# Kernel tuning notes

Measured on AMD Instinct MI355X. Metric: run time of the kernel, lower is better.

The kernel has to match this reference:

```python
import jax, jax.numpy as jnp
import numpy as np

SB_EPSILON = 0.1
SB_SIZE = 1

B, S, L = 16, 256, 24


def _shift(x, axis, k):
    """y[..., i, ...] = x[..., i + k, ...], zero-padded out of range."""
    if k == 0:
        return x
    n = x.shape[axis]
    if k > 0:
        body = jax.lax.slice_in_dim(x, k, n, axis=axis)
        pad = jnp.zeros_like(jax.lax.slice_in_dim(x, 0, k, axis=axis))
        return jnp.concatenate([body, pad], axis=axis)
    k = -k
    body = jax.lax.slice_in_dim(x, 0, n - k, axis=axis)
    pad = jnp.zeros_like(jax.lax.slice_in_dim(x, 0, k, axis=axis))
    return jnp.concatenate([pad, body], axis=axis)


def setup_inputs() -> dict:
    key = jax.random.key(0)
    k1, k2 = jax.random.split(key)
    predict = jax.random.normal(k1, (B, S, S, L), dtype=jnp.float32)
    target = (jax.random.uniform(k2, (B, S, S, L)) < 0.002).astype(jnp.float32)
    # valid spans: end >= start
    tri = (jnp.arange(S)[None, :] >= jnp.arange(S)[:, None]).astype(jnp.int32)
    mask = jnp.broadcast_to(tri[None, :, :, None], (B, S, S, L)).astype(jnp.int32)
    # keep targets only on valid spans
    target = target * mask.astype(jnp.float32)
    return {"predict": predict, "target": target, "mask": mask}


def reference(predict, target, mask):
    dt = predict.dtype
    P = (target == 1).astype(dt)            # positive spans [B,S,S,L]
    M = (mask == 1).astype(dt)              # valid-span mask
    # subtract full epsilon from each positive span
    b2l = jnp.where(target == 1, target - SB_EPSILON, target)
    for dist in range(1, SB_SIZE + 1):
        eps = SB_EPSILON / (SB_SIZE * dist * 4)
        cnt = jnp.zeros_like(P)   # num valid neighbors per positive span
        add = jnp.zeros_like(P)   # smoothing mass scattered onto neighbors
        # NOTE: original code offsets neighbors by sb_size (not dist); identical for sb_size=1
        for axis, k in ((2, SB_SIZE), (2, -SB_SIZE), (1, SB_SIZE), (1, -SB_SIZE)):
            cnt = cnt + _shift(M, axis, k)          # neighbor in range and mask==1
            add = add + _shift(P, axis, -k)         # positives scattering into this cell
        b2l = b2l + eps * (add * M + P * (dist * 4 - cnt))
    # masked BCE-with-logits, mean over mask==1 elements
    x, t = predict, b2l
    bce = jnp.maximum(x, 0) - x * t + jnp.log1p(jnp.exp(-jnp.abs(x)))
    denom = jnp.sum(M)
    return jnp.sum(bce * M) / denom
```

## Files before the change

### kernel.cpp

```cpp
#include <hip/hip_runtime.h>


#define SS 256
#define LL 24

typedef float    fvec4 __attribute__((ext_vector_type(4)));
typedef unsigned uvec4 __attribute__((ext_vector_type(4)));

constexpr float    EPS4      = 0.025f;
constexpr float    INV_DENOM = 1.0f / 12632064.0f;
constexpr int      NT        = 256;
constexpr int      NB        = 2048;
constexpr unsigned PERB6     = 197376u;
constexpr unsigned TOT6      = 16u * PERB6;
constexpr unsigned STRIDE    = (unsigned)(NB * NT);
constexpr float    LOG2E     = 1.4426950408889634f;
constexpr float    LN2       = 0.6931471805599453f;

__device__ __forceinline__ int tri_prefix(int i) {
    return (i * (513 - i)) >> 1;
}

__device__ __forceinline__ int decode_q(unsigned u, int& i_out, int& j_out) {
    unsigned b = u / PERB6;
    unsigned r = u - b * PERB6;
    unsigned c = r / 6u;
    unsigned m = r - c * 6u;
    float disc = (float)(263169u - 8u * c);
    int i = (int)((513.0f - sqrtf(disc)) * 0.5f);
    if (tri_prefix(i) > (int)c) --i;
    if (tri_prefix(i + 1) <= (int)c) ++i;
    int j = i + ((int)c - tri_prefix(i));
    i_out = i;
    j_out = j;
    return (int)(((b << 8) + (unsigned)i) * 256u + (unsigned)j) * 6 + (int)m;
}

__device__ __forceinline__ float sp_part(float x) {
    float u = __builtin_amdgcn_exp2f(-LOG2E * fabsf(x));
    return fmaxf(x, 0.f) + LN2 * __builtin_amdgcn_logf(1.f + u);
}

__device__ __forceinline__ void process(const fvec4& x, const uvec4& t,
                                        int i, int j, int q,
                                        const float* __restrict__ predf,
                                        float& acc, float& corr) {
    acc += sp_part(x.x) + sp_part(x.y) + sp_part(x.z) + sp_part(x.w);

    if ((t.x | t.y | t.z | t.w) != 0u) {
        bool hasL = j > i;
        bool hasR = j < SS - 1;
        bool hasU = i > 0;
        float cnt = (hasL ? 2.f : 0.f) + (hasR ? 1.f : 0.f) + (hasU ? 1.f : 0.f);
        int ebase = q * 4;
        unsigned tu[4] = {t.x, t.y, t.z, t.w};
        float    xv[4] = {x.x, x.y, x.z, x.w};
#pragma unroll
        for (int k = 0; k < 4; ++k) {
            if (tu[k] != 0u) {
                int e = ebase + k;
                float s = 0.f;
                if (hasL) s += predf[e - LL];
                if (hasR) s += predf[e + LL];
                if (hasU) s += predf[e - LL * SS];
                if (hasL) s += predf[e + LL * SS];
                corr += fmaf(EPS4, s - xv[k] * cnt, xv[k]);
            }
        }
    }
}

__global__ __launch_bounds__(NT) void bs_flat(const fvec4* __restrict__ pred4,
                                              const uvec4* __restrict__ targ4,
                                              const float* __restrict__ predf,
                                              float* __restrict__ partial) {
    float acc  = 0.f;
    float corr = 0.f;

    unsigned u0 = blockIdx.x * NT + threadIdx.x;
    int i0, j0;
    int q0 = decode_q(u0, i0, j0);
    fvec4 x0 = __builtin_nontemporal_load(pred4 + q0);
    uvec4 t0 = __builtin_nontemporal_load(targ4 + q0);

    unsigned u1 = u0 + STRIDE;
    bool m1 = u1 < TOT6;
    int i1 = 0, j1 = 0, q1 = 0; fvec4 x1; uvec4 t1;
    if (m1) {
        q1 = decode_q(u1, i1, j1);
        x1 = __builtin_nontemporal_load(pred4 + q1);
        t1 = __builtin_nontemporal_load(targ4 + q1);
    }

    for (;;) {
        unsigned u2 = u0 + 2 * STRIDE;
        bool m2 = u2 < TOT6;
        int i2 = 0, j2 = 0, q2 = 0; fvec4 x2; uvec4 t2;
        if (m2) {
            q2 = decode_q(u2, i2, j2);
            x2 = __builtin_nontemporal_load(pred4 + q2);
            t2 = __builtin_nontemporal_load(targ4 + q2);
        }

        process(x0, t0, i0, j0, q0, predf, acc, corr);

        if (!m1) break;
        u0 = u1; q0 = q1; i0 = i1; j0 = j1; x0 = x1; t0 = t1;
        u1 = u2; q1 = q2; i1 = i2; j1 = j2; x1 = x2; t1 = t2;
        m1 = m2;
    }

    float vsum = acc - corr;

#pragma unroll
    for (int off = 32; off; off >>= 1) vsum += __shfl_down(vsum, off, 64);
    __shared__ float s[NT / 64];
    int w = threadIdx.x >> 6;
    if ((threadIdx.x & 63) == 0) s[w] = vsum;
    __syncthreads();
    if (threadIdx.x == 0) {
        float bsum = 0.f;
#pragma unroll
        for (int k = 0; k < NT / 64; ++k) bsum += s[k];
        partial[blockIdx.x] = bsum;
    }
}

__global__ __launch_bounds__(256) void bs_final(const float* __restrict__ partial,
                                                float* __restrict__ out) {
    float acc = 0.f;
#pragma unroll
    for (int k = threadIdx.x; k < NB; k += 256) acc += partial[k];
#pragma unroll
    for (int off = 32; off; off >>= 1) acc += __shfl_down(acc, off, 64);
    __shared__ float s[4];
    int w = threadIdx.x >> 6;
    if ((threadIdx.x & 63) == 0) s[w] = acc;
    __syncthreads();
    if (threadIdx.x == 0)
        out[0] = (s[0] + s[1] + s[2] + s[3]) * INV_DENOM;
}

extern "C" void kernel_launch(void* const* d_in, const int* in_sizes, int n_in,
                              void* d_out, int out_size, void* d_ws, size_t ws_size,
                              hipStream_t stream) {
    const fvec4* pred4 = (const fvec4*)d_in[0];
    const uvec4* targ4 = (const uvec4*)d_in[1];
    const float* predf = (const float*)d_in[0];
    float* partial = (float*)d_ws;
    float* out     = (float*)d_out;

    bs_flat <<<NB, NT, 0, stream>>>(pred4, targ4, predf, partial);
    bs_final<<<1, 256, 0, stream>>>(partial, out);
}
```

Before: 234.8 us.

## Fuse final reduction into main kernel via last-block atomic counter

Replaces the separate final-reduction kernel with a last-block-done pattern: each block writes its partial, bumps an atomic counter, and the last block sums all partials and writes the output. The grid is also shrunk from 2048 to 512 blocks, so each thread loops over more elements and there are fewer partials to combine. This removes one kernel launch but adds a memset before the kernel, and the smaller grid may leave fewer waves in flight to hide memory latency.

```diff
diff --git a/kernel.cpp b/kernel.cpp
--- a/kernel.cpp
+++ b/kernel.cpp
@@ -10,10 +10,10 @@
 constexpr float    EPS4      = 0.025f;
 constexpr float    INV_DENOM = 1.0f / 12632064.0f;
 constexpr int      NT        = 256;
-constexpr int      NB        = 2048;
+constexpr int      NBLK      = 512;
 constexpr unsigned PERB6     = 197376u;
 constexpr unsigned TOT6      = 16u * PERB6;
-constexpr unsigned STRIDE    = (unsigned)(NB * NT);
+constexpr unsigned STRIDE    = (unsigned)(NBLK * NT);
 constexpr float    LOG2E     = 1.4426950408889634f;
 constexpr float    LN2       = 0.6931471805599453f;
 
@@ -70,10 +70,12 @@
     }
 }
 
-__global__ __launch_bounds__(NT) void bs_flat(const fvec4* __restrict__ pred4,
-                                              const uvec4* __restrict__ targ4,
-                                              const float* __restrict__ predf,
-                                              float* __restrict__ partial) {
+__global__ __launch_bounds__(NT) void bs_fused(const fvec4* __restrict__ pred4,
+                                               const uvec4* __restrict__ targ4,
+                                               const float* __restrict__ predf,
+                                               float* __restrict__ partial,
+                                               unsigned*    __restrict__ counter,
+                                               float*       __restrict__ out) {
     float acc  = 0.f;
     float corr = 0.f;
 
@@ -115,6 +117,7 @@
 #pragma unroll
     for (int off = 32; off; off >>= 1) vsum += __shfl_down(vsum, off, 64);
     __shared__ float s[NT / 64];
+    __shared__ bool  last;
     int w = threadIdx.x >> 6;
     if ((threadIdx.x & 63) == 0) s[w] = vsum;
     __syncthreads();
@@ -123,22 +126,24 @@
 #pragma unroll
         for (int k = 0; k < NT / 64; ++k) bsum += s[k];
         partial[blockIdx.x] = bsum;
+        __threadfence();
+        unsigned n = atomicAdd(counter, 1u);
+        last = (n == (unsigned)(NBLK - 1));
     }
-}
+    __syncthreads();
 
-__global__ __launch_bounds__(256) void bs_final(const float* __restrict__ partial,
-                                                float* __restrict__ out) {
-    float acc = 0.f;
+    if (last) {
+        __threadfence();
+        volatile const float* vp = partial;
+        float a = 0.f;
+        for (int k = threadIdx.x; k < NBLK; k += NT) a += vp[k];
 #pragma unroll
-    for (int k = threadIdx.x; k < NB; k += 256) acc += partial[k];
-#pragma unroll
-    for (int off = 32; off; off >>= 1) acc += __shfl_down(acc, off, 64);
-    __shared__ float s[4];
-    int w = threadIdx.x >> 6;
-    if ((threadIdx.x & 63) == 0) s[w] = acc;
-    __syncthreads();
-    if (threadIdx.x == 0)
-        out[0] = (s[0] + s[1] + s[2] + s[3]) * INV_DENOM;
+        for (int off = 32; off; off >>= 1) a += __shfl_down(a, off, 64);
+        if ((threadIdx.x & 63) == 0) s[w] = a;
+        __syncthreads();
+        if (threadIdx.x == 0)
+            out[0] = (s[0] + s[1] + s[2] + s[3]) * INV_DENOM;
+    }
 }
 
 extern "C" void kernel_launch(void* const* d_in, const int* in_sizes, int n_in,
@@ -147,9 +152,10 @@
     const fvec4* pred4 = (const fvec4*)d_in[0];
     const uvec4* targ4 = (const uvec4*)d_in[1];
     const float* predf = (const float*)d_in[0];
-    float* partial = (float*)d_ws;
-    float* out     = (float*)d_out;
+    float*    partial = (float*)d_ws;
+    unsigned* counter = (unsigned*)((char*)d_ws + NBLK * sizeof(float));
+    float*    out     = (float*)d_out;
 
-    bs_flat <<<NB, NT, 0, stream>>>(pred4, targ4, predf, partial);
-    bs_final<<<1, 256, 0, stream>>>(partial, out);
+    hipMemsetAsync(counter, 0, sizeof(unsigned), stream);
+    bs_fused<<<NBLK, NT, 0, stream>>>(pred4, targ4, predf, partial, counter, out);
 }
```

Result: slower. 270.8 us (+15.4%).
